# Kernel tuning notes

Measured on AMD Instinct MI355X. Metric: run time of the kernel, lower is better.

## Reference

```python
import jax, jax.numpy as jnp
import numpy as np
from jax import lax

B, V, N = 32, 3, 128          # batch, views, worm points
H, W = 512, 512               # image_size
DECAY_FACTOR = 10.0           # MAX_DECAY_FACTOR buffer value
OOB = 1e-05                   # oob_grad_val
MAX_STEPS = 10
LR, ALPHA, EPS = 0.2, 0.99, 1e-08  # torch.optim.RMSprop defaults (lr=0.2)

_b = jnp.arange(B)[:, None, None]   # (B,1,1)
_c = jnp.arange(V)[None, :, None]   # (1,3,1)


def _get_yx(p):
    # round -> long -> clamp to [0, H-1]; col 1 is y (row), col 0 is x (col)
    pi = jnp.clip(jnp.round(p).astype(jnp.int32), 0, H - 1)
    return pi[..., 1], pi[..., 0]  # each (B,3,N)


def _points_to_masks(p):
    y, x = _get_yx(p)
    return jnp.zeros((B, V, H, W), jnp.float32).at[_b, _c, y, x].set(1.0)


def _gradient_surface(masks_diff):
    grad0 = -masks_diff  # (B,3,H,W)
    grads = [grad0]
    g = grad0
    while g.shape[-1] > 1:
        gp = jnp.pad(g, ((0, 0), (0, 0), (1, 1), (1, 1)), constant_values=OOB)
        g = lax.reduce_window(gp, 0.0, lax.add, (1, 1, 3, 3), (1, 1, 2, 2), 'VALID') / 9.0
        grads.append(g)
    gs = jnp.zeros_like(grad0)
    for g in grads:
        # F.interpolate bilinear align_corners=False == jax.image.resize 'linear'
        gs = gs + jax.image.resize(g, grad0.shape, 'linear')
    ga = gs / len(grads)
    gapx = jnp.pad(ga, ((0, 0), (0, 0), (1, 1), (0, 0)), mode='edge')
    gx = (gapx[:, :, :-2] - gapx[:, :, 2:]) * 0.5   # central diff along H
    gapy = jnp.pad(ga, ((0, 0), (0, 0), (0, 0), (1, 1)), mode='edge')
    gy = (gapy[..., :-2] - gapy[..., 2:]) * 0.5     # central diff along W
    return jnp.stack([gx, gy])  # (2,B,3,H,W)


def setup_inputs() -> dict:
    key = jax.random.key(0)
    k1, k2 = jax.random.split(key)
    points_2d = jax.random.uniform(k1, (B, V, N, 2), jnp.float32) * (H - 1)
    masks_target = jax.random.uniform(k2, (B, V, H, W), jnp.float32)
    return {'points_2d': points_2d, 'masks_target': masks_target}


def reference(points_2d, masks_target):
    decay = jnp.exp(-jnp.arange(N, dtype=jnp.float32) / N * DECAY_FACTOR)  # (N,)
    masks_out = _points_to_masks(points_2d)
    masks_diff = masks_target - 0.01 * masks_out
    J = _gradient_surface(masks_diff)  # (2,B,3,H,W)
    p0 = lax.stop_gradient(points_2d)  # matches .clone().detach()

    def body(carry, _):
        p, sq, done = carry
        y, x = _get_yx(p)
        pl = (1.0 - masks_target[_b, _c, y, x]) * decay  # (B,3,N)
        cont = pl.max() > 0.1
        active = jnp.logical_and(jnp.logical_not(done), cont)
        gxp = J[0][_b, _c, y, x]
        gyp = J[1][_b, _c, y, x]
        g = -jnp.stack([gyp, gxp], axis=-1) * pl[..., None]  # (B,3,N,2)
        # RMSprop step
        sq_n = ALPHA * sq + (1.0 - ALPHA) * g * g
        p_n = p - LR * g / (jnp.sqrt(sq_n) + EPS)
        p = jnp.where(active, p_n, p)
        sq = jnp.where(active, sq_n, sq)
        done = jnp.logical_or(done, jnp.logical_not(cont))
        return (p, sq, done), None

    (p_opt, _, _), _ = lax.scan(body, (p0, jnp.zeros_like(p0), jnp.array(False)), None, length=MAX_STEPS)
    masks_opt = _points_to_masks(p_opt)
    return masks_out, masks_opt, p_opt
```

## Files before the change

kernel.cpp:

```cpp
#include <hip/hip_runtime.h>

#define IMGS 96
#define HW   262144
#define NPTS 12288
#define OOBV 1e-5f

static constexpr size_t PYR_OFF   = 0;
static constexpr size_t PFIN_OFF  = 8388576;
static constexpr size_t PLMAX_OFF = 8413152;
static constexpr size_t CNT_OFF   = 8413163;
static constexpr size_t LIST_OFF  = 8413164;
static constexpr size_t GA_OFF    = 8425472;

__device__ __forceinline__ int clampi(int v, int lo, int hi) {
    v = v < lo ? lo : v;
    return v > hi ? hi : v;
}

__global__ void k_scatter(const float* __restrict__ pts, float* __restrict__ mo,
                          int* __restrict__ cnt, int* __restrict__ plist) {
    int i = blockIdx.x * blockDim.x + threadIdx.x;
    if (i >= NPTS) return;
    float px = pts[2*i], py = pts[2*i+1];
    int xi = clampi((int)rintf(px), 0, 511);
    int yi = clampi((int)rintf(py), 0, 511);
    int gp = (i >> 7) * HW + yi * 512 + xi;
    float old = atomicExch(&mo[gp], 1.0f);
    if (old == 0.0f) {
        int k = atomicAdd(cnt, 1);
        plist[k] = gp;
    }
}

__global__ void k_lvl1(const float* __restrict__ mt, float* __restrict__ out) {
    int t = blockIdx.x * blockDim.x + threadIdx.x;
    if (t >= IMGS * 65536) return;
    int j = t & 255, i = (t >> 8) & 255, img = t >> 16;
    const float* m = mt + (size_t)img * HW;
    float s = 0.0f;
    #pragma unroll
    for (int dy = -1; dy <= 1; ++dy) {
        int y = 2*i + dy;
        #pragma unroll
        for (int dx = -1; dx <= 1; ++dx) {
            int x = 2*j + dx;
            s += (y >= 0 && y < 512 && x >= 0 && x < 512) ? -m[y*512 + x] : OOBV;
        }
    }
    out[t] = s / 9.0f;
}

__global__ void k_corr1(const int* __restrict__ cnt, const int* __restrict__ plist,
                        float* __restrict__ lvl1) {
    int k = blockIdx.x * blockDim.x + threadIdx.x;
    if (k >= *cnt) return;
    int gp = plist[k];
    int img = gp >> 18;
    int r = gp & (HW - 1);
    int y = r >> 9, x = r & 511;
    float* L = lvl1 + (size_t)img * 65536;
    const float c = 0.01f / 9.0f;
    int ilo = y >> 1, ihi = ((y + 1) >> 1) > 255 ? 255 : ((y + 1) >> 1);
    int jlo = x >> 1, jhi = ((x + 1) >> 1) > 255 ? 255 : ((x + 1) >> 1);
    for (int i = ilo; i <= ihi; ++i)
        for (int j = jlo; j <= jhi; ++j)
            atomicAdd(&L[i*256 + j], c);
}

__global__ void k_lvl2(const float* __restrict__ in, float* __restrict__ out) {
    int t = blockIdx.x * blockDim.x + threadIdx.x;
    if (t >= IMGS * 16384) return;
    int j = t & 127, i = (t >> 7) & 127, img = t >> 14;
    const float* m = in + (size_t)img * 65536;
    float s = 0.0f;
    #pragma unroll
    for (int dy = -1; dy <= 1; ++dy) {
        int y = 2*i + dy;
        #pragma unroll
        for (int dx = -1; dx <= 1; ++dx) {
            int x = 2*j + dx;
            s += (y >= 0 && y < 256 && x >= 0 && x < 256) ? m[y*256 + x] : OOBV;
        }
    }
    out[t] = s / 9.0f;
}

__global__ __launch_bounds__(256) void k_pyrtail(float* __restrict__ pyr) {
    __shared__ float buf[5461];
    int img = blockIdx.x;
    const float* L2 = pyr + 6291456 + (size_t)img * 16384;
    for (int t = threadIdx.x; t < 4096; t += 256) {
        int i = t >> 6, j = t & 63;
        float s = 0.0f;
        #pragma unroll
        for (int dy = -1; dy <= 1; ++dy) {
            int y = 2*i + dy;
            #pragma unroll
            for (int dx = -1; dx <= 1; ++dx) {
                int x = 2*j + dx;
                s += (y >= 0 && y < 128 && x >= 0 && x < 128) ? L2[y*128 + x] : OOBV;
            }
        }
        float v = s / 9.0f;
        buf[t] = v;
        pyr[7864320 + (size_t)img * 4096 + t] = v;
    }
    __syncthreads();
    int inOff = 0, sin = 64;
    size_t goff = 8257536;
    while (sin > 1) {
        int sout = sin >> 1;
        int outOff = inOff + sin * sin;
        for (int t = threadIdx.x; t < sout * sout; t += 256) {
            int i = t / sout, j = t - i * sout;
            float s = 0.0f;
            for (int dy = -1; dy <= 1; ++dy) {
                int y = 2*i + dy;
                for (int dx = -1; dx <= 1; ++dx) {
                    int x = 2*j + dx;
                    s += (y >= 0 && y < sin && x >= 0 && x < sin) ? buf[inOff + y*sin + x] : OOBV;
                }
            }
            float v = s / 9.0f;
            buf[outOff + t] = v;
            pyr[goff + (size_t)img * sout * sout + t] = v;
        }
        __syncthreads();
        inOff = outOff; sin = sout;
        goff += (size_t)96 * sout * sout;
    }
}

__global__ __launch_bounds__(256) void k_ga(const float* __restrict__ mt,
                                            const float* __restrict__ pyr,
                                            float* __restrict__ ga) {
    __shared__ float vrow[520];
    int img = blockIdx.x >> 9;
    int h = blockIdx.x & 511;
    float hf = (float)h;

    for (int e = threadIdx.x; e < 520; e += 256) {
        int l = 0, rem = e;
        while (true) {
            int len = (256 >> l) + 1;
            if (rem < len) break;
            rem -= len; ++l;
        }
        int s = 256 >> l;
        int x = rem < s ? rem : s - 1;
        float scale = (float)s * (1.0f / 512.0f);
        float fy = (hf + 0.5f) * scale - 0.5f;
        fy = fminf(fmaxf(fy, 0.0f), (float)(s - 1));
        float fyf = floorf(fy);
        int y0 = (int)fyf;
        float ty = fy - fyf;
        int yb = (y0 + 1 < s) ? y0 + 1 : s - 1;
        const float* Lp = pyr + (8388608 - (8388608 >> (2*l))) + (size_t)img * s * s;
        float a = Lp[y0*s + x], b = Lp[yb*s + x];
        vrow[e] = (1.0f - ty) * a + ty * b;
    }
    __syncthreads();

    #pragma unroll
    for (int rep = 0; rep < 2; ++rep) {
        int w = threadIdx.x + rep * 256;
        int idx = img * HW + h * 512 + w;
        float wf = (float)w;
        float acc = -mt[idx];
        #pragma unroll
        for (int l = 0; l < 9; ++l) {
            const int s = 256 >> l;
            const float scale = (float)s * (1.0f / 512.0f);
            float fx = (wf + 0.5f) * scale - 0.5f;
            fx = fminf(fmaxf(fx, 0.0f), (float)(s - 1));
            float fxf = floorf(fx);
            int x0 = (int)fxf;
            float tx = fx - fxf;
            const int vo = 512 - (512 >> l) + l;
            float a = vrow[vo + x0], b = vrow[vo + x0 + 1];
            acc += (1.0f - tx) * a + tx * b;
        }
        ga[idx] = acc / 10.0f;
    }
}

__global__ void k_corrga(const int* __restrict__ cnt, const int* __restrict__ plist,
                         float* __restrict__ ga) {
    int k = blockIdx.x * blockDim.x + threadIdx.x;
    if (k >= *cnt) return;
    ga[plist[k]] += 0.001f;
}

__global__ __launch_bounds__(256) void k_traj(const float* __restrict__ pts,
                                              const float* __restrict__ mt,
                                              const float* __restrict__ ga,
                                              float* __restrict__ pfin,
                                              float* __restrict__ plmax) {
    int i = blockIdx.x * 256 + threadIdx.x;
    float px = pts[2*i], py = pts[2*i+1];
    int img = i >> 7, n = i & 127;
    const float* M = mt + (size_t)img * HW;
    const float* G = ga + (size_t)img * HW;
    float d = expf(-(float)n * 0.078125f);
    float s0 = 0.0f, s1 = 0.0f;

    for (int t = 0; t < 10; ++t) {
        int xi = clampi((int)rintf(px), 0, 511);
        int yi = clampi((int)rintf(py), 0, 511);
        float pl = (1.0f - M[yi*512 + xi]) * d;
        float r = pl;
        #pragma unroll
        for (int off = 32; off; off >>= 1) r = fmaxf(r, __shfl_xor(r, off, 64));
        if ((threadIdx.x & 63) == 0)
            atomicMax((int*)&plmax[t], __float_as_int(r));
        float gxp = (G[clampi(yi-1,0,511)*512 + xi] - G[clampi(yi+1,0,511)*512 + xi]) * 0.5f;
        float gyp = (G[yi*512 + clampi(xi-1,0,511)] - G[yi*512 + clampi(xi+1,0,511)]) * 0.5f;
        float g0 = -gyp * pl;
        float g1 = -gxp * pl;
        s0 = 0.99f * s0 + 0.01f * g0 * g0;
        s1 = 0.99f * s1 + 0.01f * g1 * g1;
        px = px - 0.2f * g0 / (sqrtf(s0) + 1e-8f);
        py = py - 0.2f * g1 / (sqrtf(s1) + 1e-8f);
    }
    pfin[2*i] = px; pfin[2*i+1] = py;
}

__global__ __launch_bounds__(256) void k_fix(const float* __restrict__ pts,
                                             const float* __restrict__ mt,
                                             const float* __restrict__ ga,
                                             float* __restrict__ pfin,
                                             const float* __restrict__ plmax) {
    int tstop = 10;
    for (int t = 0; t < 10; ++t) {
        if (!(plmax[t] > 0.1f)) { tstop = t; break; }
    }
    if (tstop == 10) return;
    int i = blockIdx.x * 256 + threadIdx.x;
    float px = pts[2*i], py = pts[2*i+1];
    int img = i >> 7, n = i & 127;
    const float* M = mt + (size_t)img * HW;
    const float* G = ga + (size_t)img * HW;
    float d = expf(-(float)n * 0.078125f);
    float s0 = 0.0f, s1 = 0.0f;
    for (int t = 0; t < tstop; ++t) {
        int xi = clampi((int)rintf(px), 0, 511);
        int yi = clampi((int)rintf(py), 0, 511);
        float pl = (1.0f - M[yi*512 + xi]) * d;
        float gxp = (G[clampi(yi-1,0,511)*512 + xi] - G[clampi(yi+1,0,511)*512 + xi]) * 0.5f;
        float gyp = (G[yi*512 + clampi(xi-1,0,511)] - G[yi*512 + clampi(xi+1,0,511)]) * 0.5f;
        float g0 = -gyp * pl;
        float g1 = -gxp * pl;
        s0 = 0.99f * s0 + 0.01f * g0 * g0;
        s1 = 0.99f * s1 + 0.01f * g1 * g1;
        px = px - 0.2f * g0 / (sqrtf(s0) + 1e-8f);
        py = py - 0.2f * g1 / (sqrtf(s1) + 1e-8f);
    }
    pfin[2*i] = px; pfin[2*i+1] = py;
}

__global__ void k_final(const float* __restrict__ p, float* __restrict__ mopt,
                        float* __restrict__ pout) {
    int i = blockIdx.x * blockDim.x + threadIdx.x;
    if (i >= NPTS) return;
    float px = p[2*i], py = p[2*i+1];
    pout[2*i] = px; pout[2*i+1] = py;
    int xi = clampi((int)rintf(px), 0, 511);
    int yi = clampi((int)rintf(py), 0, 511);
    mopt[(i >> 7) * HW + yi*512 + xi] = 1.0f;
}

extern "C" void kernel_launch(void* const* d_in, const int* in_sizes, int n_in,
                              void* d_out, int out_size, void* d_ws, size_t ws_size,
                              hipStream_t stream) {
    const float* pts = (const float*)d_in[0];
    const float* mt  = (const float*)d_in[1];
    if (in_sizes[0] != NPTS * 2) { const float* tmp = pts; pts = mt; mt = tmp; }

    float* out  = (float*)d_out;
    float* mo   = out;
    float* mopt = out + (size_t)IMGS * HW;
    float* pout = out + 2 * (size_t)IMGS * HW;

    float* ws    = (float*)d_ws;
    float* pyr   = ws + PYR_OFF;
    float* pfin  = ws + PFIN_OFF;
    float* plmax = ws + PLMAX_OFF;
    int*   cnt   = (int*)(ws + CNT_OFF);
    int*   plist = (int*)(ws + LIST_OFF);
    float* ga    = ws + GA_OFF;

    hipMemsetAsync(out, 0, (size_t)out_size * sizeof(float), stream);
    hipMemsetAsync(plmax, 0, 12 * sizeof(float), stream);

    k_scatter<<<NPTS/256, 256, 0, stream>>>(pts, mo, cnt, plist);
    k_lvl1<<<IMGS*65536/256, 256, 0, stream>>>(mt, pyr);
    k_corr1<<<NPTS/256, 256, 0, stream>>>(cnt, plist, pyr);
    k_lvl2<<<IMGS*16384/256, 256, 0, stream>>>(pyr, pyr + 6291456);
    k_pyrtail<<<IMGS, 256, 0, stream>>>(pyr);
    k_ga<<<IMGS*512, 256, 0, stream>>>(mt, pyr, ga);
    k_corrga<<<NPTS/256, 256, 0, stream>>>(cnt, plist, ga);
    k_traj<<<NPTS/256, 256, 0, stream>>>(pts, mt, ga, pfin, plmax);
    k_fix<<<NPTS/256, 256, 0, stream>>>(pts, mt, ga, pfin, plmax);
    k_final<<<NPTS/256, 256, 0, stream>>>(pfin, mopt, pout);
}
```

Measured before the change: 433.5 us.

## Process eight rows per block in k_ga and fuse fix with final kernel

k_ga now handles 8 output rows per block. It precomputes the per-column bilinear indices and weights once in registers and reuses them across the rows, with a larger shared staging buffer holding all 8 vertically-interpolated rows. This cuts the block count 8x and amortizes index math and launch overhead. The k_fix recompute path is merged into k_final, removing one kernel launch. The trade is more registers and shared memory per block and fewer blocks in flight.

Result: no change. 426.9 us (-1.5%).

```diff
diff --git a/kernel.cpp b/kernel.cpp
--- a/kernel.cpp
+++ b/kernel.cpp
@@ -134,39 +134,38 @@
 __global__ __launch_bounds__(256) void k_ga(const float* __restrict__ mt,
                                             const float* __restrict__ pyr,
                                             float* __restrict__ ga) {
-    __shared__ float vrow[520];
-    int img = blockIdx.x >> 9;
-    int h = blockIdx.x & 511;
-    float hf = (float)h;
-
-    for (int e = threadIdx.x; e < 520; e += 256) {
-        int l = 0, rem = e;
-        while (true) {
-            int len = (256 >> l) + 1;
-            if (rem < len) break;
-            rem -= len; ++l;
-        }
-        int s = 256 >> l;
-        int x = rem < s ? rem : s - 1;
-        float scale = (float)s * (1.0f / 512.0f);
-        float fy = (hf + 0.5f) * scale - 0.5f;
-        fy = fminf(fmaxf(fy, 0.0f), (float)(s - 1));
-        float fyf = floorf(fy);
-        int y0 = (int)fyf;
-        float ty = fy - fyf;
-        int yb = (y0 + 1 < s) ? y0 + 1 : s - 1;
+    __shared__ float vrow[8][520];
+    int img = blockIdx.x >> 6;
+    int h0 = (blockIdx.x & 63) * 8;
+
+    #pragma unroll
+    for (int l = 0; l < 9; ++l) {
+        const int s = 256 >> l;
+        const int vo = 512 - (512 >> l) + l;
+        const float scale = (float)s * (1.0f / 512.0f);
         const float* Lp = pyr + (8388608 - (8388608 >> (2*l))) + (size_t)img * s * s;
-        float a = Lp[y0*s + x], b = Lp[yb*s + x];
-        vrow[e] = (1.0f - ty) * a + ty * b;
+        for (int e = threadIdx.x; e < 8*(s+1); e += 256) {
+            int r = e / (s+1);
+            int x = e - r*(s+1);
+            int xx = x < s ? x : s - 1;
+            float hf = (float)(h0 + r);
+            float fy = (hf + 0.5f) * scale - 0.5f;
+            fy = fminf(fmaxf(fy, 0.0f), (float)(s - 1));
+            float fyf = floorf(fy);
+            int y0 = (int)fyf;
+            float ty = fy - fyf;
+            int yb = (y0 + 1 < s) ? y0 + 1 : s - 1;
+            float a = Lp[y0*s + xx], b = Lp[yb*s + xx];
+            vrow[r][vo + x] = (1.0f - ty) * a + ty * b;
+        }
     }
     __syncthreads();
 
+    int   x0v[2][9];
+    float txv[2][9];
     #pragma unroll
     for (int rep = 0; rep < 2; ++rep) {
-        int w = threadIdx.x + rep * 256;
-        int idx = img * HW + h * 512 + w;
-        float wf = (float)w;
-        float acc = -mt[idx];
+        float wf = (float)(threadIdx.x + rep * 256);
         #pragma unroll
         for (int l = 0; l < 9; ++l) {
             const int s = 256 >> l;
@@ -174,13 +173,27 @@
             float fx = (wf + 0.5f) * scale - 0.5f;
             fx = fminf(fmaxf(fx, 0.0f), (float)(s - 1));
             float fxf = floorf(fx);
-            int x0 = (int)fxf;
-            float tx = fx - fxf;
-            const int vo = 512 - (512 >> l) + l;
-            float a = vrow[vo + x0], b = vrow[vo + x0 + 1];
-            acc += (1.0f - tx) * a + tx * b;
-        }
-        ga[idx] = acc / 10.0f;
+            x0v[rep][l] = (int)fxf + (512 - (512 >> l) + l);
+            txv[rep][l] = fx - fxf;
+        }
+    }
+
+    for (int r = 0; r < 8; ++r) {
+        int h = h0 + r;
+        #pragma unroll
+        for (int rep = 0; rep < 2; ++rep) {
+            int w = threadIdx.x + rep * 256;
+            int idx = img * HW + h * 512 + w;
+            float acc = -mt[idx];
+            #pragma unroll
+            for (int l = 0; l < 9; ++l) {
+                float a = vrow[r][x0v[rep][l]];
+                float b = vrow[r][x0v[rep][l] + 1];
+                float tx = txv[rep][l];
+                acc += (1.0f - tx) * a + tx * b;
+            }
+            ga[idx] = acc / 10.0f;
+        }
     }
 }
 
@@ -225,44 +238,42 @@
     pfin[2*i] = px; pfin[2*i+1] = py;
 }
 
-__global__ __launch_bounds__(256) void k_fix(const float* __restrict__ pts,
-                                             const float* __restrict__ mt,
-                                             const float* __restrict__ ga,
-                                             float* __restrict__ pfin,
-                                             const float* __restrict__ plmax) {
+__global__ __launch_bounds__(256) void k_final(const float* __restrict__ pts,
+                                               const float* __restrict__ mt,
+                                               const float* __restrict__ ga,
+                                               const float* __restrict__ pfin,
+                                               const float* __restrict__ plmax,
+                                               float* __restrict__ mopt,
+                                               float* __restrict__ pout) {
     int tstop = 10;
-    for (int t = 0; t < 10; ++t) {
-        if (!(plmax[t] > 0.1f)) { tstop = t; break; }
-    }
-    if (tstop == 10) return;
+    #pragma unroll
+    for (int t = 9; t >= 0; --t)
+        if (!(plmax[t] > 0.1f)) tstop = t;
     int i = blockIdx.x * 256 + threadIdx.x;
-    float px = pts[2*i], py = pts[2*i+1];
-    int img = i >> 7, n = i & 127;
-    const float* M = mt + (size_t)img * HW;
-    const float* G = ga + (size_t)img * HW;
-    float d = expf(-(float)n * 0.078125f);
-    float s0 = 0.0f, s1 = 0.0f;
-    for (int t = 0; t < tstop; ++t) {
-        int xi = clampi((int)rintf(px), 0, 511);
-        int yi = clampi((int)rintf(py), 0, 511);
-        float pl = (1.0f - M[yi*512 + xi]) * d;
-        float gxp = (G[clampi(yi-1,0,511)*512 + xi] - G[clampi(yi+1,0,511)*512 + xi]) * 0.5f;
-        float gyp = (G[yi*512 + clampi(xi-1,0,511)] - G[yi*512 + clampi(xi+1,0,511)]) * 0.5f;
-        float g0 = -gyp * pl;
-        float g1 = -gxp * pl;
-        s0 = 0.99f * s0 + 0.01f * g0 * g0;
-        s1 = 0.99f * s1 + 0.01f * g1 * g1;
-        px = px - 0.2f * g0 / (sqrtf(s0) + 1e-8f);
-        py = py - 0.2f * g1 / (sqrtf(s1) + 1e-8f);
-    }
-    pfin[2*i] = px; pfin[2*i+1] = py;
-}
-
-__global__ void k_final(const float* __restrict__ p, float* __restrict__ mopt,
-                        float* __restrict__ pout) {
-    int i = blockIdx.x * blockDim.x + threadIdx.x;
-    if (i >= NPTS) return;
-    float px = p[2*i], py = p[2*i+1];
+    float px, py;
+    if (tstop == 10) {
+        px = pfin[2*i]; py = pfin[2*i+1];
+    } else {
+        px = pts[2*i]; py = pts[2*i+1];
+        int img = i >> 7, n = i & 127;
+        const float* M = mt + (size_t)img * HW;
+        const float* G = ga + (size_t)img * HW;
+        float d = expf(-(float)n * 0.078125f);
+        float s0 = 0.0f, s1 = 0.0f;
+        for (int t = 0; t < tstop; ++t) {
+            int xi = clampi((int)rintf(px), 0, 511);
+            int yi = clampi((int)rintf(py), 0, 511);
+            float pl = (1.0f - M[yi*512 + xi]) * d;
+            float gxp = (G[clampi(yi-1,0,511)*512 + xi] - G[clampi(yi+1,0,511)*512 + xi]) * 0.5f;
+            float gyp = (G[yi*512 + clampi(xi-1,0,511)] - G[yi*512 + clampi(xi+1,0,511)]) * 0.5f;
+            float g0 = -gyp * pl;
+            float g1 = -gxp * pl;
+            s0 = 0.99f * s0 + 0.01f * g0 * g0;
+            s1 = 0.99f * s1 + 0.01f * g1 * g1;
+            px = px - 0.2f * g0 / (sqrtf(s0) + 1e-8f);
+            py = py - 0.2f * g1 / (sqrtf(s1) + 1e-8f);
+        }
+    }
     pout[2*i] = px; pout[2*i+1] = py;
     int xi = clampi((int)rintf(px), 0, 511);
     int yi = clampi((int)rintf(py), 0, 511);
@@ -297,9 +308,8 @@
     k_corr1<<<NPTS/256, 256, 0, stream>>>(cnt, plist, pyr);
     k_lvl2<<<IMGS*16384/256, 256, 0, stream>>>(pyr, pyr + 6291456);
     k_pyrtail<<<IMGS, 256, 0, stream>>>(pyr);
-    k_ga<<<IMGS*512, 256, 0, stream>>>(mt, pyr, ga);
+    k_ga<<<IMGS*64, 256, 0, stream>>>(mt, pyr, ga);
     k_corrga<<<NPTS/256, 256, 0, stream>>>(cnt, plist, ga);
     k_traj<<<NPTS/256, 256, 0, stream>>>(pts, mt, ga, pfin, plmax);
-    k_fix<<<NPTS/256, 256, 0, stream>>>(pts, mt, ga, pfin, plmax);
-    k_final<<<NPTS/256, 256, 0, stream>>>(pfin, mopt, pout);
-}
+    k_final<<<NPTS/256, 256, 0, stream>>>(pts, mt, ga, pfin, plmax, mopt, pout);
+}
```
